# Kernel tuning notes

Hardware: AMD Instinct MI355X
Metric: run time of the kernel (lower is better)

Reference implementation:

```python
import jax, jax.numpy as jnp
import numpy as np

N, E, DIMS, IN_C, OUT_C = 50000, 800000, 5, 32, 32
NEG_SLOPE = 0.2


def setup_inputs() -> dict:
    key = jax.random.key(0)
    k1, k2, k3, k4, k5 = jax.random.split(key, 5)
    x = jax.random.normal(k1, (N, IN_C * DIMS), dtype=jnp.float32)
    edge_index = jax.random.randint(k2, (2, E), 0, N, dtype=jnp.int64)
    edge_attr = jax.random.normal(k3, (E, DIMS), dtype=jnp.float32)
    # per-dim EGATConv parameters, stacked over dims (heads=1, concat=False)
    W = jax.random.normal(k4, (DIMS, IN_C, OUT_C), dtype=jnp.float32) / np.sqrt(IN_C).astype(np.float32)
    att = jax.random.normal(k5, (DIMS, 2 * OUT_C + 1), dtype=jnp.float32) / np.sqrt(2 * OUT_C + 1).astype(np.float32)
    return {"x": x, "edge_index": edge_index, "edge_attr": edge_attr, "W": W, "att": att}


def reference(x, edge_index, edge_attr, W, att):
    n = x.shape[0]
    dims, out_c = W.shape[0], W.shape[2]
    # x.reshape(N, -1, dims): per-dim feature slice, then per-dim linear projection
    xr = x.reshape(n, -1, dims)                      # [N, IN_C, dims]
    h = jnp.einsum('nid,dio->ndo', xr, W)            # [N, dims, OUT_C]
    row, col = edge_index[0], edge_index[1]
    h_i = h[row]                                     # [E, dims, OUT_C] target
    h_j = h[col]                                     # [E, dims, OUT_C] source
    att_i = att[:, :out_c]                           # [dims, OUT_C]
    att_j = att[:, out_c:2 * out_c]                  # [dims, OUT_C]
    att_e = att[:, -1]                               # [dims]
    # attention logits from cat([h_i, h_j, edge_attr]) . att, per edge, per dim
    score = (jnp.einsum('edo,do->ed', h_i, att_i)
             + jnp.einsum('edo,do->ed', h_j, att_j)
             + edge_attr * att_e)                    # [E, dims]
    score = jax.nn.leaky_relu(score, NEG_SLOPE)
    # scatter-softmax over incoming edges of each target node
    smax = jax.lax.stop_gradient(jax.ops.segment_max(score, row, num_segments=n))
    escore = jnp.exp(score - smax[row])
    ssum = jax.ops.segment_sum(escore, row, num_segments=n)
    alpha = escore / (ssum[row] + 1e-16)             # [E, dims]
    # scatter-add aggregation of alpha-weighted source features
    out = jax.ops.segment_sum(alpha[:, :, None] * h_j, row, num_segments=n)  # [N, dims, OUT_C]
    out = out.reshape(n, dims * out_c)               # torch.cat(out_l, dim=-1)
    return out, alpha, edge_index
```

## Files before the change

### kernel.cpp

```cpp
#include <hip/hip_runtime.h>
#include <hip/hip_bf16.h>
#include <math.h>

#define N_NODES 50000
#define N_EDGES 800000
#define DIMS 5
#define IN_C 32
#define OUT_C 32
#define FEAT 160
#define ATT_LD 65
#define NEG_SLOPE 0.2f
#define BSHIFT 7
#define BROWS 128
#define NBUCK ((N_NODES + BROWS - 1) / BROWS)
#define CAP 2560
#define K1_EPB 4096
#define K1_BLOCKS ((N_EDGES + K1_EPB - 1) / K1_EPB)

__global__ __launch_bounds__(1024) void hist_kernel(
        const int* __restrict__ ei, float* __restrict__ fedge,
        int* __restrict__ ghist, unsigned short* __restrict__ lofs) {
    __shared__ int hist[NBUCK];
    int blk = blockIdx.x, t = threadIdx.x;
    if (t < NBUCK) hist[t] = 0;
    __syncthreads();
#pragma unroll
    for (int u = 0; u < 4; ++u) {
        int e = blk * K1_EPB + u * 1024 + t;
        if (e < N_EDGES) {
            int r = ei[e];
            int c = ei[N_EDGES + e];
            __builtin_nontemporal_store((float)r, &fedge[e]);
            __builtin_nontemporal_store((float)c, &fedge[N_EDGES + e]);
            int b = r >> BSHIFT;
            int lo = atomicAdd(&hist[b], 1);
            lofs[e] = (unsigned short)lo;
        }
    }
    __syncthreads();
    if (t < NBUCK) ghist[blk * NBUCK + t] = hist[t];
}

__global__ void colsum_kernel(const int* __restrict__ ghist, int* __restrict__ btot) {
    __shared__ int red[256];
    int b = blockIdx.x, t = threadIdx.x;
    int s = 0;
    for (int blk = t; blk < K1_BLOCKS; blk += 256) s += ghist[blk * NBUCK + b];
    red[t] = s;
    __syncthreads();
    for (int off = 128; off > 0; off >>= 1) {
        if (t < off) red[t] += red[t + off];
        __syncthreads();
    }
    if (t == 0) btot[b] = red[0];
}

__global__ void bscan2_kernel(const int* __restrict__ btot, int* __restrict__ bbase) {
    __shared__ int buf[512];
    int t = threadIdx.x;
    int v = (t < NBUCK) ? btot[t] : 0;
    buf[t] = v;
    __syncthreads();
    for (int off = 1; off < 512; off <<= 1) {
        int add = (t >= off) ? buf[t - off] : 0;
        __syncthreads();
        buf[t] += add;
        __syncthreads();
    }
    if (t < NBUCK) bbase[t] = buf[t] - v;
}

__global__ void colscan_kernel(const int* __restrict__ ghist, const int* __restrict__ bbase,
                               int* __restrict__ base2) {
    __shared__ int buf[256];
    int b = blockIdx.x, t = threadIdx.x;
    int v = (t < K1_BLOCKS) ? ghist[t * NBUCK + b] : 0;
    buf[t] = v;
    __syncthreads();
    for (int off = 1; off < 256; off <<= 1) {
        int add = (t >= off) ? buf[t - off] : 0;
        __syncthreads();
        buf[t] += add;
        __syncthreads();
    }
    if (t < K1_BLOCKS) base2[t * NBUCK + b] = bbase[b] + buf[t] - v;
}

__global__ __launch_bounds__(1024) void place_kernel(
        const int* __restrict__ ei, const unsigned short* __restrict__ lofs,
        const int* __restrict__ base2,
        const float* __restrict__ edge_attr,
        const float* __restrict__ ai, const float* __restrict__ aj,
        const float* __restrict__ att,
        int4* __restrict__ staged) {
    __shared__ int lbase[NBUCK];
    __shared__ float satte[DIMS];
    int blk = blockIdx.x, t = threadIdx.x;
    if (t < NBUCK) lbase[t] = base2[blk * NBUCK + t];
    if (t < DIMS) satte[t] = att[t * ATT_LD + 2 * OUT_C];
    __syncthreads();
#pragma unroll
    for (int u = 0; u < 4; ++u) {
        int e = blk * K1_EPB + u * 1024 + t;
        if (e < N_EDGES) {
            int r = ei[e];
            int c = ei[N_EDGES + e];
            const float* air = ai + r * DIMS;
            const float* ajr = aj + c * DIMS;
            const float* ea  = edge_attr + (size_t)e * DIMS;
            unsigned es[DIMS];
#pragma unroll
            for (int d = 0; d < DIMS; ++d) {
                float s = air[d] + ajr[d] + ea[d] * satte[d];
                s = (s > 0.f) ? s : NEG_SLOPE * s;
                __hip_bfloat16 h = __float2bfloat16(__expf(s));
                es[d] = (unsigned)*(unsigned short*)&h;
            }
            int4 st;
            st.x = c | ((r & (BROWS - 1)) << 16);
            st.y = (int)(es[0] | (es[1] << 16));
            st.z = (int)(es[2] | (es[3] << 16));
            st.w = (int)es[4];
            staged[lbase[r >> BSHIFT] + (int)lofs[e]] = st;
        }
    }
}

__global__ __launch_bounds__(256) void build_kernel(
        const int4* __restrict__ staged, const int* __restrict__ btot,
        const int* __restrict__ bbase,
        unsigned* __restrict__ csrd, int* __restrict__ rowStart) {
    __shared__ int4 sst[CAP];
    __shared__ int rcount[BROWS];
    __shared__ int rexcl[BROWS];
    __shared__ int sbuf[BROWS];
    int b = blockIdx.x;
    int t = threadIdx.x;
    int cnt  = btot[b];
    int base = bbase[b];
    const int4* sg = staged + base;
    for (int i = t; i < cnt; i += 256) sst[i] = sg[i];
    if (t < BROWS) rcount[t] = 0;
    __syncthreads();
    for (int i = t; i < cnt; i += 256)
        atomicAdd(&rcount[((unsigned)sst[i].x >> 16) & (BROWS - 1)], 1);
    __syncthreads();
    if (t < BROWS) sbuf[t] = rcount[t];
    __syncthreads();
    for (int off = 1; off < BROWS; off <<= 1) {
        int add = (t < BROWS && t >= off) ? sbuf[t - off] : 0;
        __syncthreads();
        if (t < BROWS) sbuf[t] += add;
        __syncthreads();
    }
    if (t < BROWS) {
        rexcl[t] = sbuf[t] - rcount[t];
        int idx = b * BROWS + t;
        if (idx <= N_NODES) rowStart[idx] = base + rexcl[t];
        rcount[t] = 0;
    }
    __syncthreads();
    for (int i = t; i < cnt; i += 256) {
        int4 p = sst[i];
        int rl = ((unsigned)p.x >> 16) & (BROWS - 1);
        unsigned c = (unsigned)p.x & 0xffffu;
        int lp = atomicAdd(&rcount[rl], 1);
        int pos = base + rexcl[rl] + lp;
        unsigned es0 = (unsigned)p.y & 0xffffu;
        unsigned es1 = (unsigned)p.y >> 16;
        unsigned es2v = (unsigned)p.z & 0xffffu;
        unsigned es3 = (unsigned)p.z >> 16;
        unsigned es4 = (unsigned)p.w & 0xffffu;
        csrd[0 * N_EDGES + pos] = c | (es0 << 16);
        csrd[1 * N_EDGES + pos] = c | (es1 << 16);
        csrd[2 * N_EDGES + pos] = c | (es2v << 16);
        csrd[3 * N_EDGES + pos] = c | (es3 << 16);
        csrd[4 * N_EDGES + pos] = c | (es4 << 16);
    }
}

__global__ __launch_bounds__(256) void hfused_kernel(
        const float* __restrict__ x, const float* __restrict__ W,
        const float* __restrict__ att,
        __hip_bfloat16* __restrict__ h2,
        float* __restrict__ ai, float* __restrict__ aj) {
    __shared__ float sW[DIMS * IN_C * OUT_C];
    int tid = threadIdx.x;
    {
        const float4* Wg = (const float4*)W;
        float4* sW4 = (float4*)sW;
#pragma unroll
        for (int j = 0; j < 5; ++j)
            sW4[j * 256 + tid] = Wg[j * 256 + tid];
    }
    __syncthreads();

    int idx = blockIdx.x * 256 + tid;
    int pr = idx >> 3;
    int og = idx & 7;
    int n0 = pr * 2;
    if (n0 >= N_NODES) return;
    const float4* xr0 = (const float4*)(x + (size_t)n0 * FEAT);
    const float4* xr1 = xr0 + 40;

    float acc0[DIMS][4], acc1[DIMS][4];
#pragma unroll
    for (int d = 0; d < DIMS; ++d)
#pragma unroll
        for (int q = 0; q < 4; ++q) { acc0[d][q] = 0.f; acc1[d][q] = 0.f; }

#pragma unroll
    for (int ib = 0; ib < 8; ++ib) {
        float xs0[20], xs1[20];
#pragma unroll
        for (int q = 0; q < 5; ++q) {
            float4 v0 = xr0[ib * 5 + q];
            float4 v1 = xr1[ib * 5 + q];
            xs0[q * 4 + 0] = v0.x; xs0[q * 4 + 1] = v0.y;
            xs0[q * 4 + 2] = v0.z; xs0[q * 4 + 3] = v0.w;
            xs1[q * 4 + 0] = v1.x; xs1[q * 4 + 1] = v1.y;
            xs1[q * 4 + 2] = v1.z; xs1[q * 4 + 3] = v1.w;
        }
#pragma unroll
        for (int ii = 0; ii < 4; ++ii) {
            int i = ib * 4 + ii;
#pragma unroll
            for (int d = 0; d < DIMS; ++d) {
                float4 wv = *(const float4*)(sW + ((d * IN_C + i) * OUT_C) + og * 4);
                float xv0 = xs0[ii * 5 + d];
                float xv1 = xs1[ii * 5 + d];
                acc0[d][0] += xv0 * wv.x; acc0[d][1] += xv0 * wv.y;
                acc0[d][2] += xv0 * wv.z; acc0[d][3] += xv0 * wv.w;
                acc1[d][0] += xv1 * wv.x; acc1[d][1] += xv1 * wv.y;
                acc1[d][2] += xv1 * wv.z; acc1[d][3] += xv1 * wv.w;
            }
        }
    }

    __hip_bfloat16* hp0 = h2 + (size_t)n0 * FEAT + og * 4;
#pragma unroll
    for (int d = 0; d < DIMS; ++d) {
        union { __hip_bfloat16 h[4]; uint2 u; } pk;
        pk.h[0] = __float2bfloat16(acc0[d][0]);
        pk.h[1] = __float2bfloat16(acc0[d][1]);
        pk.h[2] = __float2bfloat16(acc0[d][2]);
        pk.h[3] = __float2bfloat16(acc0[d][3]);
        *(uint2*)(hp0 + d * OUT_C) = pk.u;
    }
    __hip_bfloat16* hp1 = hp0 + FEAT;
#pragma unroll
    for (int d = 0; d < DIMS; ++d) {
        union { __hip_bfloat16 h[4]; uint2 u; } pk;
        pk.h[0] = __float2bfloat16(acc1[d][0]);
        pk.h[1] = __float2bfloat16(acc1[d][1]);
        pk.h[2] = __float2bfloat16(acc1[d][2]);
        pk.h[3] = __float2bfloat16(acc1[d][3]);
        *(uint2*)(hp1 + d * OUT_C) = pk.u;
    }

    float pa0[DIMS], pb0[DIMS], pa1[DIMS], pb1[DIMS];
#pragma unroll
    for (int d = 0; d < DIMS; ++d) {
        const float* at = att + d * ATT_LD + og * 4;
        const float* bt = at + OUT_C;
        pa0[d] = acc0[d][0] * at[0] + acc0[d][1] * at[1] + acc0[d][2] * at[2] + acc0[d][3] * at[3];
        pb0[d] = acc0[d][0] * bt[0] + acc0[d][1] * bt[1] + acc0[d][2] * bt[2] + acc0[d][3] * bt[3];
        pa1[d] = acc1[d][0] * at[0] + acc1[d][1] * at[1] + acc1[d][2] * at[2] + acc1[d][3] * at[3];
        pb1[d] = acc1[d][0] * bt[0] + acc1[d][1] * bt[1] + acc1[d][2] * bt[2] + acc1[d][3] * bt[3];
    }
#pragma unroll
    for (int m = 1; m < 8; m <<= 1) {
#pragma unroll
        for (int d = 0; d < DIMS; ++d) {
            pa0[d] += __shfl_xor(pa0[d], m, 8);
            pb0[d] += __shfl_xor(pb0[d], m, 8);
            pa1[d] += __shfl_xor(pa1[d], m, 8);
            pb1[d] += __shfl_xor(pb1[d], m, 8);
        }
    }
    if (og == 0) {
#pragma unroll
        for (int d = 0; d < DIMS; ++d) {
            ai[n0 * DIMS + d] = pa0[d];
            aj[n0 * DIMS + d] = pb0[d];
            ai[(n0 + 1) * DIMS + d] = pa1[d];
            aj[(n0 + 1) * DIMS + d] = pb1[d];
        }
    }
}

__device__ inline float bf2f(unsigned short u) {
    return __uint_as_float(((unsigned)u) << 16);
}

__global__ __launch_bounds__(320) void out_kernel(
        const __hip_bfloat16* __restrict__ h2,
        const unsigned* __restrict__ csrd,
        const int* __restrict__ rowStart,
        float* __restrict__ out, float* __restrict__ ssum) {
    int g = threadIdx.x / 40;
    int l = threadIdx.x - g * 40;
    int node = blockIdx.x * 8 + g;
    int d = l >> 3;
    const unsigned* cs = csrd + (size_t)d * N_EDGES;
    int start = rowStart[node];
    int end   = rowStart[node + 1];
    float a0 = 0.f, a1 = 0.f, a2 = 0.f, a3 = 0.f, ss = 0.f;
    if (end > start) {
        int last = end - 1;
        int k = start;
        unsigned ceA[8];
#pragma unroll
        for (int u = 0; u < 8; ++u) {
            int kk = k + u;
            ceA[u] = cs[kk <= last ? kk : last];
        }
        while (true) {
            int kn = k + 8;
            bool more = (kn < end);
            float av[8]; uint2 hv[8]; unsigned ceB[8];
#pragma unroll
            for (int u = 0; u < 8; ++u) {
                float a = bf2f((unsigned short)(ceA[u] >> 16));
                av[u] = (k + u < end) ? a : 0.f;
            }
#pragma unroll
            for (int u = 0; u < 8; ++u)
                hv[u] = *(const uint2*)(h2 + (size_t)(ceA[u] & 0xffffu) * FEAT + l * 4);
            if (more) {
#pragma unroll
                for (int u = 0; u < 8; ++u) {
                    int kk = kn + u;
                    ceB[u] = cs[kk <= last ? kk : last];
                }
            }
#pragma unroll
            for (int u = 0; u < 8; ++u) {
                float a = av[u];
                ss += a;
                a0 += a * __uint_as_float(hv[u].x << 16);
                a1 += a * __uint_as_float(hv[u].x & 0xffff0000u);
                a2 += a * __uint_as_float(hv[u].y << 16);
                a3 += a * __uint_as_float(hv[u].y & 0xffff0000u);
            }
            if (!more) break;
            k = kn;
#pragma unroll
            for (int u = 0; u < 8; ++u) ceA[u] = ceB[u];
        }
    }
    float inv = 1.f / (ss + 1e-16f);
    union { float f[4]; unsigned long long u[2]; } o;
    o.f[0] = a0 * inv; o.f[1] = a1 * inv; o.f[2] = a2 * inv; o.f[3] = a3 * inv;
    unsigned long long* op = (unsigned long long*)(out + (size_t)node * FEAT + l * 4);
    __builtin_nontemporal_store(o.u[0], op);
    __builtin_nontemporal_store(o.u[1], op + 1);
    if ((l & 7) == 0) ssum[node * DIMS + d] = ss;
}

__global__ void alpha_kernel(const int* __restrict__ ei,
                             const float* __restrict__ edge_attr,
                             const float* __restrict__ ai, const float* __restrict__ aj,
                             const float* __restrict__ att,
                             const float* __restrict__ ssum,
                             float* __restrict__ alpha_buf) {
    int idx = blockIdx.x * blockDim.x + threadIdx.x;
    if (idx >= N_EDGES * DIMS) return;
    int e = idx / DIMS;
    int d = idx - e * DIMS;
    int r = ei[e];
    int c = ei[N_EDGES + e];
    float s = ai[r * DIMS + d] + aj[c * DIMS + d]
            + edge_attr[idx] * att[d * ATT_LD + 2 * OUT_C];
    s = (s > 0.f) ? s : NEG_SLOPE * s;
    __hip_bfloat16 h = __float2bfloat16(__expf(s));
    float a = bf2f(*(unsigned short*)&h) / (ssum[r * DIMS + d] + 1e-16f);
    __builtin_nontemporal_store(a, &alpha_buf[idx]);
}

extern "C" void kernel_launch(void* const* d_in, const int* in_sizes, int n_in,
                              void* d_out, int out_size, void* d_ws, size_t ws_size,
                              hipStream_t stream) {
    const float* x         = (const float*)d_in[0];
    const int*   ei        = (const int*)d_in[1];
    const float* edge_attr = (const float*)d_in[2];
    const float* W         = (const float*)d_in[3];
    const float* att       = (const float*)d_in[4];

    float* out_buf   = (float*)d_out;
    float* alpha_buf = out_buf + (size_t)N_NODES * FEAT;
    float* fedge     = alpha_buf + (size_t)N_EDGES * DIMS;

    int4* staged = (int4*)alpha_buf;
    unsigned short* lofs = (unsigned short*)((char*)alpha_buf + 12800000);

    char* wsb = (char*)d_ws;
    __hip_bfloat16* h2 = (__hip_bfloat16*)wsb;
    float* ai     = (float*)(wsb + 16000000);
    float* aj     = (float*)(wsb + 17000000);
    float* ssum   = (float*)(wsb + 18000000);
    unsigned* csrd = (unsigned*)(wsb + 19000000);
    int* ghist    = (int*)(wsb + 35000000);
    int* base2    = (int*)(wsb + 35310000);
    int* btot     = (int*)(wsb + 35620000);
    int* bbase    = (int*)(wsb + 35622000);
    int* rowStart = (int*)(wsb + 35624000);

    const int B = 256;

    hist_kernel<<<K1_BLOCKS, 1024, 0, stream>>>(ei, fedge, ghist, lofs);
    hfused_kernel<<<(N_NODES / 2 * 8 + B - 1) / B, B, 0, stream>>>(x, W, att, h2, ai, aj);
    colsum_kernel<<<NBUCK, 256, 0, stream>>>(ghist, btot);
    bscan2_kernel<<<1, 512, 0, stream>>>(btot, bbase);
    colscan_kernel<<<NBUCK, 256, 0, stream>>>(ghist, bbase, base2);
    place_kernel<<<K1_BLOCKS, 1024, 0, stream>>>(ei, lofs, base2, edge_attr,
                                                 ai, aj, att, staged);
    build_kernel<<<NBUCK, 256, 0, stream>>>(staged, btot, bbase, csrd, rowStart);
    out_kernel<<<N_NODES / 8, 320, 0, stream>>>(h2, csrd, rowStart, out_buf, ssum);
    alpha_kernel<<<(N_EDGES * DIMS + B - 1) / B, B, 0, stream>>>(ei, edge_attr, ai, aj, att,
                                                                 ssum, alpha_buf);
}
```

Measured before the change: 152.1 us.

## Stage bucketed edges in shared memory before coalesced global scatter

The place kernel now sorts each block's 4096 edges by bucket in shared memory, using a per-block exclusive scan of the block histogram. It then writes them out in bucket-sorted order, so consecutive threads write contiguous runs into each bucket's staged region instead of scattering 16-byte records randomly. This adds 64KB of shared memory per block plus a 512-wide scan with many barriers, which may reduce occupancy. The bucket id is packed into the high bits of the column word (c < 65536, bucket < 391 fits in 9 bits).

```diff
diff --git a/kernel.cpp b/kernel.cpp
--- a/kernel.cpp
+++ b/kernel.cpp
@@ -88,23 +88,42 @@
 
 __global__ __launch_bounds__(1024) void place_kernel(
         const int* __restrict__ ei, const unsigned short* __restrict__ lofs,
-        const int* __restrict__ base2,
+        const int* __restrict__ base2, const int* __restrict__ ghist,
         const float* __restrict__ edge_attr,
         const float* __restrict__ ai, const float* __restrict__ aj,
         const float* __restrict__ att,
         int4* __restrict__ staged) {
+    __shared__ int4 sstg[K1_EPB];
     __shared__ int lbase[NBUCK];
+    __shared__ int lexcl[NBUCK];
+    __shared__ int sbuf[512];
     __shared__ float satte[DIMS];
     int blk = blockIdx.x, t = threadIdx.x;
     if (t < NBUCK) lbase[t] = base2[blk * NBUCK + t];
     if (t < DIMS) satte[t] = att[t * ATT_LD + 2 * OUT_C];
-    __syncthreads();
+    if (t < 512) sbuf[t] = (t < NBUCK) ? ghist[blk * NBUCK + t] : 0;
+    __syncthreads();
+    int v = (t < 512) ? sbuf[t] : 0;
+    for (int off = 1; off < 512; off <<= 1) {
+        int add = (t < 512 && t >= off) ? sbuf[t - off] : 0;
+        __syncthreads();
+        if (t < 512) sbuf[t] += add;
+        __syncthreads();
+    }
+    if (t < NBUCK) lexcl[t] = sbuf[t] - v;
+    __syncthreads();
+
+    int ebase = blk * K1_EPB;
+    int cnt2 = N_EDGES - ebase; if (cnt2 > K1_EPB) cnt2 = K1_EPB;
+
 #pragma unroll
     for (int u = 0; u < 4; ++u) {
-        int e = blk * K1_EPB + u * 1024 + t;
-        if (e < N_EDGES) {
+        int i = u * 1024 + t;
+        if (i < cnt2) {
+            int e = ebase + i;
             int r = ei[e];
             int c = ei[N_EDGES + e];
+            int b = r >> BSHIFT;
             const float* air = ai + r * DIMS;
             const float* ajr = aj + c * DIMS;
             const float* ea  = edge_attr + (size_t)e * DIMS;
@@ -117,11 +136,21 @@
                 es[d] = (unsigned)*(unsigned short*)&h;
             }
             int4 st;
-            st.x = c | ((r & (BROWS - 1)) << 16);
+            st.x = c | ((r & (BROWS - 1)) << 16) | (b << 23);
             st.y = (int)(es[0] | (es[1] << 16));
             st.z = (int)(es[2] | (es[3] << 16));
             st.w = (int)es[4];
-            staged[lbase[r >> BSHIFT] + (int)lofs[e]] = st;
+            sstg[lexcl[b] + (int)lofs[e]] = st;
+        }
+    }
+    __syncthreads();
+#pragma unroll
+    for (int u = 0; u < 4; ++u) {
+        int i = u * 1024 + t;
+        if (i < cnt2) {
+            int4 p = sstg[i];
+            int b = (unsigned)p.x >> 23;
+            staged[lbase[b] + (i - lexcl[b])] = p;
         }
     }
 }
@@ -413,7 +442,7 @@
     colsum_kernel<<<NBUCK, 256, 0, stream>>>(ghist, btot);
     bscan2_kernel<<<1, 512, 0, stream>>>(btot, bbase);
     colscan_kernel<<<NBUCK, 256, 0, stream>>>(ghist, bbase, base2);
-    place_kernel<<<K1_BLOCKS, 1024, 0, stream>>>(ei, lofs, base2, edge_attr,
+    place_kernel<<<K1_BLOCKS, 1024, 0, stream>>>(ei, lofs, base2, ghist, edge_attr,
                                                  ai, aj, att, staged);
     build_kernel<<<NBUCK, 256, 0, stream>>>(staged, btot, bbase, csrd, rowStart);
     out_kernel<<<N_NODES / 8, 320, 0, stream>>>(h2, csrd, rowStart, out_buf, ssum);
```

Result: faster. 146.7 us, median of 2 (-3.5%).
